# Performance work log

Measured on AMD Instinct MI355X. Metric: run time of the kernel, lower is better.

## Reference

```python
import jax, jax.numpy as jnp
import numpy as np

N_ATOMS = 256
N_FEATURES = 128
BATCH = 8
BINS = 300


def _segments(n, length=1):
    # all pairs of non-overlapping length-`length` segments: rows [i, i+L, j, j+L], j >= i+L+1
    m = n - length
    i, j = np.triu_indices(m, k=length + 1)
    return np.stack([i, i + length, j, j + length], axis=1).astype(np.int32)  # (Nseg, 4)


SEGMENTS_NP = _segments(N_ATOMS)
NSEG = SEGMENTS_NP.shape[0]  # 32131 for n_atoms=256
# edges: segment start-pairs and end-pairs, shape (2, 2*Nseg), then offset per frame
_edges_base = np.concatenate([SEGMENTS_NP[:, [0, 2]], SEGMENTS_NP[:, [1, 3]]], axis=0).T
EDGES_NP = np.concatenate([b * N_ATOMS + _edges_base for b in range(BATCH)], axis=1)  # (2, B*2*Nseg)
SRC = jnp.asarray(EDGES_NP[0].astype(np.int32))
DST = jnp.asarray(EDGES_NP[1].astype(np.int32))
SEGMENTS = jnp.asarray(SEGMENTS_NP)
BIN_CENTERS = jnp.linspace(-1.0, 1.0, BINS, dtype=jnp.float32)
STEP = 2.0 / (BINS - 1)  # linear (non-gaussian) binning: scalar step


def _divnorm(x):
    return x / jnp.linalg.norm(x, axis=-1, keepdims=True)


def _writhe_segments_cross(xyz, seg):
    # xyz: (B, N, 3), seg: (S, 4) -> writhe per segment pair (B, S)
    B, S = xyz.shape[0], seg.shape[0]
    # dx[b, s, k]: broadcasted differences xyz[seg[2+q]] - xyz[seg[p]], k = 2*p+q
    dx = (-xyz[:, seg[:, :2], None] + xyz[:, seg[:, None, 2:]]).reshape(B, S, 4, 3)
    dx = _divnorm(dx)
    crosses = _divnorm(jnp.cross(dx[:, :, [0, 1, 3, 2]], dx[:, :, [1, 3, 2, 0]]))
    dots = jnp.clip(jnp.sum(crosses * crosses[:, :, [1, 2, 3, 0]], axis=-1), -1.0, 1.0)
    omega = jnp.arcsin(dots).sum(axis=2)  # (B, S)
    signs = jnp.sign(jnp.sum(
        jnp.cross(xyz[:, seg[:, 3]] - xyz[:, seg[:, 2]], xyz[:, seg[:, 1]] - xyz[:, seg[:, 0]]) * dx[:, :, 0],
        axis=-1))
    return omega * signs / (2.0 * jnp.pi)


def setup_inputs() -> dict:
    key = jax.random.key(0)
    k1, k2, k3 = jax.random.split(key, 3)
    coords = jax.random.normal(k1, (BATCH * N_ATOMS, 3), jnp.float32)
    node_features = jax.random.normal(k2, (BATCH * N_ATOMS, N_FEATURES), jnp.float32)
    std = 1.0 / np.sqrt(N_FEATURES)
    basis = jax.random.uniform(k3, (BINS, N_FEATURES), jnp.float32, -std, std)
    return {"coords": coords, "node_features": node_features, "basis": basis}


def reference(coords, node_features, basis):
    xyz = coords.reshape(BATCH, N_ATOMS, 3)
    wr = _writhe_segments_cross(xyz, SEGMENTS)  # (B, Nseg)
    # Gaussian RBF soft one-hot over linear bins, then project onto learned basis
    enc = jnp.exp(-(((wr[..., None] - BIN_CENTERS) / STEP) ** 2)) / 1.12  # (B, S, bins)
    emb = jnp.einsum('bsk,kf->bsf', enc, basis)  # (B, S, F)
    # repeat(1,2,1): each segment pair contributes two edges (start-pair, end-pair)
    writhe_feat = jnp.tile(emb, (1, 2, 1)).reshape(-1, N_FEATURES)  # (B*2S, F)
    # distance attention: exp(-||r_src - r_dst||^2), softmax-normalized per destination node
    w = jnp.exp(-jnp.sum((coords[SRC] - coords[DST]) ** 2, axis=-1))  # (E,)
    denom = jax.ops.segment_sum(w, DST, num_segments=BATCH * N_ATOMS)
    attn = (w / denom[DST])[:, None]
    message = jax.ops.segment_sum(writhe_feat * attn, DST, num_segments=BATCH * N_ATOMS)
    return node_features + message
```

## Files before the change

kernel.cpp:

```cpp
#include <hip/hip_runtime.h>
#include <math.h>

#define N_ATOMS 256
#define N_FEAT  128
#define BATCH   8
#define BINS    300
#define INV_STEP 149.5f
#define ONE_OVER_2PI 0.15915494309189535f
#define INV_112 0.8928571428571429f
#define WIN 2
#define WINW 5
#define NHIST 8

struct V3 { float x, y, z; };
__device__ __forceinline__ V3 v3sub(V3 a, V3 b) { return {a.x-b.x, a.y-b.y, a.z-b.z}; }
__device__ __forceinline__ float v3dot(V3 a, V3 b) { return a.x*b.x + a.y*b.y + a.z*b.z; }
__device__ __forceinline__ V3 v3cross(V3 a, V3 b) {
    return {a.y*b.z - a.z*b.y, a.z*b.x - a.x*b.z, a.x*b.y - a.y*b.x};
}
__device__ __forceinline__ V3 v3nrm(V3 a) {
    float r = __builtin_amdgcn_rsqf(v3dot(a, a));
    return {a.x*r, a.y*r, a.z*r};
}
__device__ __forceinline__ float clamp1(float x) { return fminf(1.0f, fmaxf(-1.0f, x)); }

__device__ __forceinline__ float asin_fast(float x) {
    float u = fabsf(x);
    bool big = u > 0.5f;
    float z = big ? 0.5f * (1.0f - u) : u * u;
    float s = big ? __builtin_amdgcn_sqrtf(z) : u;
    float p = fmaf(z, 4.2163199048e-2f, 2.4181311049e-2f);
    p = fmaf(z, p, 4.5470025998e-2f);
    p = fmaf(z, p, 7.4953002686e-2f);
    p = fmaf(z, p, 1.6666752422e-1f);
    float r = fmaf(s * z, p, s);
    r = big ? (1.5707963267948966f - 2.0f * r) : r;
    return copysignf(r, x);
}

__device__ __forceinline__ float writhe_ij(const float* cs, int i, int j) {
    V3 pi  = {cs[i*3+0],     cs[i*3+1],     cs[i*3+2]};
    V3 pi1 = {cs[(i+1)*3+0], cs[(i+1)*3+1], cs[(i+1)*3+2]};
    V3 pj  = {cs[j*3+0],     cs[j*3+1],     cs[j*3+2]};
    V3 pj1 = {cs[(j+1)*3+0], cs[(j+1)*3+1], cs[(j+1)*3+2]};

    V3 d0 = v3nrm(v3sub(pj,  pi));
    V3 d1 = v3nrm(v3sub(pj1, pi));
    V3 d2 = v3nrm(v3sub(pj,  pi1));
    V3 d3 = v3nrm(v3sub(pj1, pi1));

    V3 c0 = v3nrm(v3cross(d0, d1));
    V3 c1 = v3nrm(v3cross(d1, d3));
    V3 c2 = v3nrm(v3cross(d3, d2));
    V3 c3 = v3nrm(v3cross(d2, d0));

    float omega = asin_fast(clamp1(v3dot(c0, c1)))
                + asin_fast(clamp1(v3dot(c1, c2)))
                + asin_fast(clamp1(v3dot(c2, c3)))
                + asin_fast(clamp1(v3dot(c3, c0)));

    float sg = v3dot(v3cross(v3sub(pj1, pj), v3sub(pi1, pi)), d0);
    float sign = (sg > 0.0f) ? 1.0f : ((sg < 0.0f) ? -1.0f : 0.0f);
    return omega * sign * ONE_OVER_2PI;
}

__global__ __launch_bounds__(512) void fused_kernel(const float* __restrict__ coords,
                                                    const float* __restrict__ nf,
                                                    const float* __restrict__ basis,
                                                    float* __restrict__ out) {
    const int blk = blockIdx.x;
    const int b = blk & 7;
    const int p = blk >> 3;
    const int t0 = p + 2;
    const int t1 = 255 - p;
    const int tid = threadIdx.x;

    const int E0  = 2 * t0 - 3;
    const int E1n = (t1 == 255) ? 253 : 2 * t1 - 3;

    float mynf = 0.0f;
    if (tid < 256) {
        const int row = (tid >> 7) ? t1 : t0;
        mynf = nf[((size_t)((b << 8) | row)) * N_FEAT + (tid & 127)];
    }

    __shared__ float cs[N_ATOMS * 3];
    __shared__ float h2[2 * NHIST * BINS];
    __shared__ float part[4 * N_FEAT];
    __shared__ float sden[2];
    __shared__ int skmin[2], skmax[2];

    for (int idx = tid; idx < N_ATOMS * 3; idx += 512)
        cs[idx] = coords[(b << 8) * 3 + idx];
    for (int k = tid; k < 2 * NHIST * BINS; k += 512) h2[k] = 0.0f;
    if (tid < 2) { sden[tid] = 0.0f; skmin[tid] = BINS - 1; skmax[tid] = 0; }
    __syncthreads();

    int node = -1;
    int tau = t0;
    if (tid < E0) { node = 0; tau = t0; }
    else if (tid < E0 + E1n) { node = 1; tau = t1; }
    const int ee = (node == 1) ? tid - E0 : tid;

    float d0 = 0.0f, d1 = 0.0f;
    int kn0 = BINS - 1, kx0 = 0, kn1 = BINS - 1, kx1 = 0;

    if (node >= 0) {
        const int eT1 = (tau <= N_ATOMS - 2) ? tau - 1 : 0;
        const int typ = (ee < eT1) ? 0 : 1;
        const int a = (typ == 0) ? ee : ee - eT1 + 1;

        float dx = cs[a*3+0] - cs[tau*3+0];
        float dy = cs[a*3+1] - cs[tau*3+1];
        float dz = cs[a*3+2] - cs[tau*3+2];
        float g = __expf(-(dx*dx + dy*dy + dz*dz));

        float w = (typ == 0) ? writhe_ij(cs, a, tau) : writhe_ij(cs, a - 1, tau - 1);
        float pp = (w + 1.0f) * INV_STEP;
        int k0 = __float2int_rn(pp);
        int kmn = max(0, k0 - WIN);
        int kmx = min(BINS - 1, k0 + WIN);
        if (node == 0) { d0 = g; kn0 = kmn; kx0 = kmx; }
        else           { d1 = g; kn1 = kmn; kx1 = kmx; }

        const int copy = tid & (NHIST - 1);
        const int rot = tid % WINW;
        const int base = (node * NHIST + copy) * BINS;
        const int klo = k0 - WIN;
        #pragma unroll
        for (int m = 0; m < WINW; ++m) {
            int mm = m + rot; if (mm >= WINW) mm -= WINW;
            int k = klo + mm;
            if (k >= 0 && k < BINS) {
                float dd = pp - (float)k;
                atomicAdd(&h2[base + k], g * __expf(-dd * dd));
            }
        }
    }

    #pragma unroll
    for (int off = 32; off > 0; off >>= 1) {
        d0 += __shfl_xor(d0, off, 64);
        d1 += __shfl_xor(d1, off, 64);
        kn0 = min(kn0, __shfl_xor(kn0, off, 64));
        kx0 = max(kx0, __shfl_xor(kx0, off, 64));
        kn1 = min(kn1, __shfl_xor(kn1, off, 64));
        kx1 = max(kx1, __shfl_xor(kx1, off, 64));
    }
    if ((tid & 63) == 0) {
        atomicAdd(&sden[0], d0);
        atomicAdd(&sden[1], d1);
        atomicMin(&skmin[0], kn0);
        atomicMax(&skmax[0], kx0);
        atomicMin(&skmin[1], kn1);
        atomicMax(&skmax[1], kx1);
    }
    __syncthreads();

    {
        const int nu = tid >> 8;
        const int kmin = skmin[nu], kmax = skmax[nu];
        const int base = nu * NHIST * BINS;
        for (int k = kmin + (tid & 255); k <= kmax; k += 256) {
            float s = h2[base + k];
            #pragma unroll
            for (int c = 1; c < NHIST; ++c) s += h2[base + c * BINS + k];
            h2[base + k] = s;
        }
    }
    __syncthreads();

    {
        const int nu = tid >> 8;
        const int h = (tid >> 7) & 1;
        const int f = tid & 127;
        const int kmin = skmin[nu], kmax = skmax[nu];
        const int len = kmax - kmin + 1;
        const int half = (len + 1) >> 1;
        const int ks = kmin + h * half;
        const int ke = min(kmax + 1, ks + half);
        const int base = nu * NHIST * BINS;
        float acc = 0.0f;
        for (int k = ks; k < ke; ++k)
            acc = fmaf(h2[base + k], basis[k * N_FEAT + f], acc);
        part[((nu << 1) | h) * N_FEAT + f] = acc;
    }
    __syncthreads();

    if (tid < 256) {
        const int nu = tid >> 7;
        const int f = tid & 127;
        const int row = nu ? t1 : t0;
        const float scale = INV_112 / sden[nu];
        const float s = part[(nu << 1) * N_FEAT + f] + part[((nu << 1) | 1) * N_FEAT + f];
        out[((size_t)((b << 8) | row)) * N_FEAT + f] = mynf + s * scale;
    } else if (p == 0) {
        const int tid2 = tid - 256;
        const int r = tid2 >> 7;
        const int f = tid2 & 127;
        const size_t idx = ((size_t)((b << 8) | r)) * N_FEAT + f;
        out[idx] = nf[idx];
    }
}

extern "C" void kernel_launch(void* const* d_in, const int* in_sizes, int n_in,
                              void* d_out, int out_size, void* d_ws, size_t ws_size,
                              hipStream_t stream) {
    const float* coords = (const float*)d_in[0];
    const float* nf     = (const float*)d_in[1];
    const float* basis  = (const float*)d_in[2];
    float* out = (float*)d_out;

    fused_kernel<<<BATCH * 127, 512, 0, stream>>>(coords, nf, basis, out);
}
```

Measured before the change: 104.9 us.

## Pair adjacent destination nodes so shared writhe values are computed once

Each block now handles two adjacent destination atoms (w, w+1) instead of a mirrored pair (t0, 255-t0). Segment pairs whose writhe feeds both nodes are computed once and scattered to both histograms, which cuts the number of writhe evaluations per block. Blocks are interleaved small/large via the q-to-p mapping to balance load, and threads loop over edges with a stride so a block can take more than 512 edges. The cost is extra branching, a second atomic per bin for shared edges, and per-block work that is less uniform than before.

```diff
diff --git a/kernel.cpp b/kernel.cpp
--- a/kernel.cpp
+++ b/kernel.cpp
@@ -64,23 +64,32 @@
     return omega * sign * ONE_OVER_2PI;
 }
 
+__device__ __forceinline__ float gw(const float* cs, int a, int t) {
+    float dx = cs[a*3+0] - cs[t*3+0];
+    float dy = cs[a*3+1] - cs[t*3+1];
+    float dz = cs[a*3+2] - cs[t*3+2];
+    return __expf(-(dx*dx + dy*dy + dz*dz));
+}
+
 __global__ __launch_bounds__(512) void fused_kernel(const float* __restrict__ coords,
                                                     const float* __restrict__ nf,
                                                     const float* __restrict__ basis,
                                                     float* __restrict__ out) {
     const int blk = blockIdx.x;
     const int b = blk & 7;
-    const int p = blk >> 3;
-    const int t0 = p + 2;
-    const int t1 = 255 - p;
+    const int q = blk >> 3;
+    const int p = (q & 1) ? (126 - (q >> 1)) : (q >> 1);
+    const int w = 2 * p + 2;
     const int tid = threadIdx.x;
 
-    const int E0  = 2 * t0 - 3;
-    const int E1n = (t1 == 255) ? 253 : 2 * t1 - 3;
+    const int E0 = w - 2;
+    const int E1 = w - 1;
+    const int E2 = (w + 1 <= N_ATOMS - 2) ? w : 0;
+    const int E = E0 + E1 + E2;
 
     float mynf = 0.0f;
     if (tid < 256) {
-        const int row = (tid >> 7) ? t1 : t0;
+        const int row = w + (tid >> 7);
         mynf = nf[((size_t)((b << 8) | row)) * N_FEAT + (tid & 127)];
     }
 
@@ -96,44 +105,46 @@
     if (tid < 2) { sden[tid] = 0.0f; skmin[tid] = BINS - 1; skmax[tid] = 0; }
     __syncthreads();
 
-    int node = -1;
-    int tau = t0;
-    if (tid < E0) { node = 0; tau = t0; }
-    else if (tid < E0 + E1n) { node = 1; tau = t1; }
-    const int ee = (node == 1) ? tid - E0 : tid;
-
     float d0 = 0.0f, d1 = 0.0f;
     int kn0 = BINS - 1, kx0 = 0, kn1 = BINS - 1, kx1 = 0;
-
-    if (node >= 0) {
-        const int eT1 = (tau <= N_ATOMS - 2) ? tau - 1 : 0;
-        const int typ = (ee < eT1) ? 0 : 1;
-        const int a = (typ == 0) ? ee : ee - eT1 + 1;
-
-        float dx = cs[a*3+0] - cs[tau*3+0];
-        float dy = cs[a*3+1] - cs[tau*3+1];
-        float dz = cs[a*3+2] - cs[tau*3+2];
-        float g = __expf(-(dx*dx + dy*dy + dz*dz));
-
-        float w = (typ == 0) ? writhe_ij(cs, a, tau) : writhe_ij(cs, a - 1, tau - 1);
-        float pp = (w + 1.0f) * INV_STEP;
-        int k0 = __float2int_rn(pp);
-        int kmn = max(0, k0 - WIN);
-        int kmx = min(BINS - 1, k0 + WIN);
-        if (node == 0) { d0 = g; kn0 = kmn; kx0 = kmx; }
-        else           { d1 = g; kn1 = kmn; kx1 = kmx; }
-
-        const int copy = tid & (NHIST - 1);
-        const int rot = tid % WINW;
-        const int base = (node * NHIST + copy) * BINS;
+    const int copy = tid & (NHIST - 1);
+    const int rot = tid % WINW;
+    const int baseA0 = copy * BINS;
+    const int baseB  = (NHIST + copy) * BINS;
+
+    for (int e = tid; e < E; e += 512) {
+        int tau, i;
+        if (e < E0)           { tau = w - 1; i = e; }
+        else if (e < E0 + E1) { tau = w;     i = e - E0; }
+        else                  { tau = w + 1; i = e - E0 - E1; }
+
+        const float wv = writhe_ij(cs, i, tau);
+        const float pp = (wv + 1.0f) * INV_STEP;
+        const int k0 = __float2int_rn(pp);
+        const int kmn = max(0, k0 - WIN);
+        const int kmx = min(BINS - 1, k0 + WIN);
         const int klo = k0 - WIN;
+
+        const int nodeA = (tau == w + 1) ? 1 : 0;
+        const int aA = (tau == w - 1) ? i + 1 : i;
+        const float gA = gw(cs, aA, w + nodeA);
+        const bool hasB = (tau == w);
+        const float gB = hasB ? gw(cs, i + 1, w + 1) : 0.0f;
+
+        if (nodeA == 0) { d0 += gA; kn0 = min(kn0, kmn); kx0 = max(kx0, kmx); }
+        else            { d1 += gA; kn1 = min(kn1, kmn); kx1 = max(kx1, kmx); }
+        if (hasB)       { d1 += gB; kn1 = min(kn1, kmn); kx1 = max(kx1, kmx); }
+
+        const int bA = (nodeA ? baseB : baseA0);
         #pragma unroll
         for (int m = 0; m < WINW; ++m) {
             int mm = m + rot; if (mm >= WINW) mm -= WINW;
-            int k = klo + mm;
+            const int k = klo + mm;
             if (k >= 0 && k < BINS) {
-                float dd = pp - (float)k;
-                atomicAdd(&h2[base + k], g * __expf(-dd * dd));
+                const float dd = pp - (float)k;
+                const float ww = __expf(-dd * dd);
+                atomicAdd(&h2[bA + k], gA * ww);
+                if (hasB) atomicAdd(&h2[baseB + k], gB * ww);
             }
         }
     }
@@ -190,7 +201,7 @@
     if (tid < 256) {
         const int nu = tid >> 7;
         const int f = tid & 127;
-        const int row = nu ? t1 : t0;
+        const int row = w + nu;
         const float scale = INV_112 / sden[nu];
         const float s = part[(nu << 1) * N_FEAT + f] + part[((nu << 1) | 1) * N_FEAT + f];
         out[((size_t)((b << 8) | row)) * N_FEAT + f] = mynf + s * scale;
```

Measured after the change: 118.1 us. 12.6% more time.
